# Performance work log

Measured on AMD Instinct MI355X. Metric: run time of the kernel, lower is better.

Reference implementation:

```python
import jax, jax.numpy as jnp
import numpy as np
from jax import lax

VOCAB = 50000; EMB = 128; HID = 256; NL = 9; B = 128; T = 512; H = HID // 2; PAD = 0


def setup_inputs() -> dict:
    key = jax.random.key(0)
    ks = jax.random.split(key, 16)
    p = lambda k, s: jax.random.normal(k, s, jnp.float32) * 0.05
    return {
        "chars": jax.random.randint(ks[0], (B, T), 1, VOCAB),  # in [1, VOCAB) so mask fully on
        "labels": jax.random.randint(ks[1], (B, T), 0, NL),
        "emb": p(ks[2], (VOCAB, EMB)),
        "W_ih_f": p(ks[3], (4 * H, EMB)), "W_hh_f": p(ks[4], (4 * H, H)),
        "b_ih_f": p(ks[5], (4 * H,)), "b_hh_f": p(ks[6], (4 * H,)),
        "W_ih_b": p(ks[7], (4 * H, EMB)), "W_hh_b": p(ks[8], (4 * H, H)),
        "b_ih_b": p(ks[9], (4 * H,)), "b_hh_b": p(ks[10], (4 * H,)),
        "W_out": p(ks[11], (NL, HID)), "b_out": p(ks[12], (NL,)),
        "start_trans": p(ks[13], (NL,)), "end_trans": p(ks[14], (NL,)),
        "trans": p(ks[15], (NL, NL)),
    }


def _lstm(x, Wih, Whh, bih, bhh, reverse):
    # x: (B, T, D); PyTorch gate order i, f, g, o
    bsz = x.shape[0]
    h0 = jnp.zeros((bsz, H), x.dtype)
    c0 = jnp.zeros((bsz, H), x.dtype)
    b = bih + bhh

    def step(carry, xt):
        h, c = carry
        g = xt @ Wih.T + h @ Whh.T + b  # (B, 4H)
        i, f, gg, o = jnp.split(g, 4, axis=-1)
        c = jax.nn.sigmoid(f) * c + jax.nn.sigmoid(i) * jnp.tanh(gg)
        h = jax.nn.sigmoid(o) * jnp.tanh(c)
        return (h, c), h

    _, hs = lax.scan(step, (h0, c0), jnp.swapaxes(x, 0, 1), reverse=reverse)
    return jnp.swapaxes(hs, 0, 1)  # (B, T, H)


def _crf_nll(emissions, labels, mask, start, end, trans):
    # torchcrf linear-chain CRF log-likelihood, reduction='sum'
    maskf = mask.astype(emissions.dtype)
    emit = jnp.take_along_axis(emissions, labels[..., None], 2)[..., 0]  # (B, T)
    score = start[labels[:, 0]] + (emit * maskf).sum(1)
    score = score + (trans[labels[:, :-1], labels[:, 1:]] * maskf[:, 1:]).sum(1)
    last_idx = mask.sum(1).astype(jnp.int32) - 1
    last_tags = jnp.take_along_axis(labels, last_idx[:, None], 1)[:, 0]
    score = score + end[last_tags]

    # forward algorithm (log partition) as a scan over time
    alpha0 = start[None, :] + emissions[:, 0]  # (B, L)

    def step(alpha, inp):
        e_t, m_t = inp  # (B, L), (B,)
        nxt = jax.nn.logsumexp(alpha[:, :, None] + trans[None, :, :], axis=1) + e_t
        return jnp.where(m_t[:, None], nxt, alpha), None

    alpha, _ = lax.scan(step, alpha0,
                        (jnp.swapaxes(emissions, 0, 1)[1:], jnp.swapaxes(mask, 0, 1)[1:]))
    logZ = jax.nn.logsumexp(alpha + end[None, :], axis=-1)
    return -(score - logZ).sum()


def reference(chars, labels, emb, W_ih_f, W_hh_f, b_ih_f, b_hh_f,
              W_ih_b, W_hh_b, b_ih_b, b_hh_b, W_out, b_out,
              start_trans, end_trans, trans):
    x = emb[chars]  # (B, T, EMB)
    hf = _lstm(x, W_ih_f, W_hh_f, b_ih_f, b_hh_f, False)
    hb = _lstm(x, W_ih_b, W_hh_b, b_ih_b, b_hh_b, True)
    h = jnp.concatenate([hf, hb], axis=-1)  # (B, T, HID)
    emissions = h @ W_out.T + b_out  # dropout is identity in eval mode
    mask = chars != PAD
    return _crf_nll(emissions, labels, mask, start_trans, end_trans, trans)
```

## Files before the change

### kernel.cpp

```cpp
#include <hip/hip_runtime.h>

#define B_   128
#define T_   512
#define EMB_ 128
#define H_   128
#define NL_  9
#define MT_  65536

typedef __attribute__((ext_vector_type(8))) short short8v;
typedef __attribute__((ext_vector_type(4))) float float4v;

__device__ inline unsigned short f2bf(float f){
  unsigned u = __float_as_uint(f);
  u += 0x7FFFu + ((u >> 16) & 1u);
  return (unsigned short)(u >> 16);
}
__device__ inline float bf2f(unsigned short s){
  return __uint_as_float(((unsigned)s) << 16);
}
__device__ inline float vrcp(float x){ float r; asm("v_rcp_f32 %0, %1" : "=v"(r) : "v"(x)); return r; }

__device__ inline float poly_sigm(float x){
  float x2 = x * x;
  float t = fmaf(x2, 2.0833333e-3f, -2.0833333e-2f);
  t = fmaf(x2, t, 0.25f);
  return fmaf(x, t, 0.5f);
}
__device__ inline float poly_tanh(float x){
  float x2 = x * x;
  float t = fmaf(x2, 0.13333333f, -0.33333333f);
  t = fmaf(x2, t, 1.f);
  return x * t;
}
__device__ inline float lstm_cell_poly(float pi, float pf, float pg, float po, float& c){
  float iv = poly_sigm(pi);
  float fv = poly_sigm(pf);
  float gv = poly_tanh(pg);
  float ov = poly_sigm(po);
  c = fmaf(fv, c, iv * gv);
  return ov * poly_tanh(c);
}

__device__ inline void bar(){
  __builtin_amdgcn_sched_barrier(0);
  asm volatile("s_waitcnt lgkmcnt(0)" ::: "memory");
  __builtin_amdgcn_sched_barrier(0);
  __builtin_amdgcn_s_barrier();
  __builtin_amdgcn_sched_barrier(0);
}

__device__ inline void gload16(const void* g, void* l){
  __builtin_amdgcn_global_load_lds(
      (const __attribute__((address_space(1))) void*)g,
      (__attribute__((address_space(3)))       void*)l, 16, 0, 0);
}

__global__ void k0_prep(const float* __restrict__ Wihf, const float* __restrict__ Whhf,
                        const float* __restrict__ bihf, const float* __restrict__ bhhf,
                        const float* __restrict__ Wihb, const float* __restrict__ Whhb,
                        const float* __restrict__ bihb, const float* __restrict__ bhhb,
                        unsigned short* __restrict__ Wih2, unsigned short* __restrict__ Whh2,
                        float* __restrict__ biasc){
  int blk = blockIdx.x;
  int dir = blk >> 9;
  int nd  = blk & 511;
  int k   = threadIdx.x;
  int j = nd >> 2, g = nd & 3;
  int orig = g * 128 + j;
  const float* Wih = dir ? Wihb : Wihf;
  const float* Whh = dir ? Whhb : Whhf;
  Wih2[((long)(dir * 512 + nd)) * 128 + k] = f2bf(Wih[orig * EMB_ + k]);
  Whh2[((long)(dir * 512 + nd)) * 128 + k] = f2bf(Whh[orig * H_ + k]);
  if (k == 0){
    const float* bi = dir ? bihb : bihf;
    const float* bh = dir ? bhhb : bhhf;
    biasc[dir * 512 + nd] = bi[orig] + bh[orig];
  }
}

__global__ __launch_bounds__(256) void k2_gemm(const int* __restrict__ chars,
                                               const float* __restrict__ emb,
                                               const unsigned short* __restrict__ Wih2,
                                               const float* __restrict__ biasc,
                                               unsigned short* __restrict__ G){
  __shared__ unsigned short sm[2][128 * 128];
  const int tid = threadIdx.x;
  const int w = tid >> 6, l = tid & 63, r = l & 15, q = l >> 4;
  const long m0 = (long)blockIdx.x * 128;
  const int  n0 = blockIdx.y * 128;

  #pragma unroll
  for (int it = 0; it < 8; it++){
    int u = it * 256 + tid, row = u >> 4, c = u & 15, cs = c ^ (row & 7);
    int ch_ = chars[m0 + row];
    const float4* ep = (const float4*)(emb + (long)ch_ * EMB_ + cs * 8);
    float4 v0 = ep[0], v1 = ep[1];
    short8v o;
    o[0] = (short)f2bf(v0.x); o[1] = (short)f2bf(v0.y);
    o[2] = (short)f2bf(v0.z); o[3] = (short)f2bf(v0.w);
    o[4] = (short)f2bf(v1.x); o[5] = (short)f2bf(v1.y);
    o[6] = (short)f2bf(v1.z); o[7] = (short)f2bf(v1.w);
    *(short8v*)&sm[0][u * 8] = o;
  }
  #pragma unroll
  for (int it = 0; it < 8; it++){
    int u = it * 256 + tid, row = u >> 4, c = u & 15, cs = c ^ (row & 7);
    gload16(Wih2 + (long)(n0 + row) * 128 + cs * 8, &sm[1][u * 8]);
  }
  __syncthreads();

  float bias[8];
  #pragma unroll
  for (int nt = 0; nt < 8; nt++) bias[nt] = biasc[n0 + nt * 16 + r];

  short8v a[2][4];
  #pragma unroll
  for (int mt = 0; mt < 2; mt++){
    int row = 32 * w + mt * 16 + r;
    #pragma unroll
    for (int kf = 0; kf < 4; kf++){
      int ch = (kf * 4 + q) ^ (row & 7);
      a[mt][kf] = *(const short8v*)&sm[0][row * 128 + ch * 8];
    }
  }
  float4v acc[2][8];
  #pragma unroll
  for (int nt = 0; nt < 8; nt++){
    short8v bfr[4];
    int brow = nt * 16 + r;
    #pragma unroll
    for (int kf = 0; kf < 4; kf++){
      int ch = (kf * 4 + q) ^ (brow & 7);
      bfr[kf] = *(const short8v*)&sm[1][brow * 128 + ch * 8];
    }
    #pragma unroll
    for (int mt = 0; mt < 2; mt++){
      float4v z = {bias[nt], bias[nt], bias[nt], bias[nt]};
      acc[mt][nt] = z;
      #pragma unroll
      for (int kf = 0; kf < 4; kf++)
        acc[mt][nt] = __builtin_amdgcn_mfma_f32_16x16x32_bf16(a[mt][kf], bfr[kf], acc[mt][nt], 0, 0, 0);
    }
  }
  __syncthreads();
  unsigned short* gsm = &sm[0][0];
  #pragma unroll
  for (int mt = 0; mt < 2; mt++){
    #pragma unroll
    for (int nt = 0; nt < 8; nt++){
      int rowL = 32 * w + mt * 16 + q * 4;
      #pragma unroll
      for (int reg = 0; reg < 4; reg++)
        gsm[(rowL + reg) * 130 + nt * 16 + r] = f2bf(acc[mt][nt][reg]);
    }
  }
  __syncthreads();
  #pragma unroll
  for (int it = 0; it < 8; it++){
    int u = it * 256 + tid, row = u >> 4, c = u & 15;
    short8v v = *(const short8v*)&gsm[row * 130 + c * 8];
    *(short8v*)(G + (m0 + row) * 1024 + n0 + c * 8) = v;
  }
}

#define HBST 128
__global__ __launch_bounds__(1024, 1) void k3_scan4(
    const unsigned short* __restrict__ G,
    const unsigned short* __restrict__ Whh2,
    unsigned short* __restrict__ hs)
{
  const int blk = blockIdx.x;
  const int dir = blk >> 3;
  const int b0  = (blk & 7) * 16;
  const int tid = threadIdx.x;
  const int w   = tid >> 6;
  const int l   = tid & 63;
  const int r   = l & 15;
  const int q   = l >> 4;
  const int rx  = r & 7;

  __shared__ unsigned short hR[8][16 * HBST];

  short8v Wf[2][4];
  #pragma unroll
  for (int t = 0; t < 2; t++){
    const unsigned short* wp = Whh2 + ((long)(dir * 512 + 32 * w + 16 * t + r)) * 128 + q * 8;
    #pragma unroll
    for (int kf = 0; kf < 4; kf++)
      Wf[t][kf] = *(const short8v*)(wp + kf * 32);
  }
  #pragma unroll
  for (int t = 0; t < 2; t++)
    #pragma unroll
    for (int kf = 0; kf < 4; kf++)
      asm volatile("" : "+v"(Wf[t][kf]));

  for (int i = tid; i < 16 * HBST; i += 1024) hR[7][i] = 0;

  float cc0 = 0.f, cc1 = 0.f;
  const int wcs = ((w ^ rx) << 3);
  const int fii = tid >> 8, fmm = (tid >> 4) & 15, fj8 = tid & 15;
  const int fco = ((fj8 ^ (fmm & 7)) << 3);

  const long gstep = dir ? -1024L : 1024L;
  const unsigned short* gbase = G + ((long)(b0 + r) * T_ + (dir ? T_ - 1 : 0)) * 1024
                                  + dir * 512 + 32 * w + 4 * q;

#define ISSUEX(D0A, D0B, D1A, D1B, S) do{                          \
    const unsigned short* p_ = gbase + (long)(S) * gstep;          \
    D0A = *(const ushort4*)(p_);                                   \
    D0B = *(const ushort4*)(p_ + 16);                              \
    D1A = *(const ushort4*)(p_ + gstep);                           \
    D1B = *(const ushort4*)(p_ + gstep + 16);                      \
  }while(0)

#define STEPX(S, GA, GB) do{                                       \
    const int slot_r = ((S) + 7) & 7, slot_w = (S) & 7;            \
    const unsigned short* rowp = &hR[slot_r][r * HBST];            \
    short8v hf0 = *(const short8v*)(rowp + (((q     ) ^ rx) << 3));\
    short8v hf1 = *(const short8v*)(rowp + (((q +  4) ^ rx) << 3));\
    short8v hf2 = *(const short8v*)(rowp + (((q +  8) ^ rx) << 3));\
    short8v hf3 = *(const short8v*)(rowp + (((q + 12) ^ rx) << 3));\
    float4v acc0 = {bf2f((GA).x), bf2f((GA).y), bf2f((GA).z), bf2f((GA).w)}; \
    float4v acc1 = {bf2f((GB).x), bf2f((GB).y), bf2f((GB).z), bf2f((GB).w)}; \
    acc0 = __builtin_amdgcn_mfma_f32_16x16x32_bf16(Wf[0][0], hf0, acc0, 0, 0, 0); \
    acc0 = __builtin_amdgcn_mfma_f32_16x16x32_bf16(Wf[0][1], hf1, acc0, 0, 0, 0); \
    acc0 = __builtin_amdgcn_mfma_f32_16x16x32_bf16(Wf[0][2], hf2, acc0, 0, 0, 0); \
    acc0 = __builtin_amdgcn_mfma_f32_16x16x32_bf16(Wf[0][3], hf3, acc0, 0, 0, 0); \
    acc1 = __builtin_amdgcn_mfma_f32_16x16x32_bf16(Wf[1][0], hf0, acc1, 0, 0, 0); \
    acc1 = __builtin_amdgcn_mfma_f32_16x16x32_bf16(Wf[1][1], hf1, acc1, 0, 0, 0); \
    acc1 = __builtin_amdgcn_mfma_f32_16x16x32_bf16(Wf[1][2], hf2, acc1, 0, 0, 0); \
    acc1 = __builtin_amdgcn_mfma_f32_16x16x32_bf16(Wf[1][3], hf3, acc1, 0, 0, 0); \
    float hv0 = lstm_cell_poly(acc0[0], acc0[1], acc0[2], acc0[3], cc0);\
    float hv1 = lstm_cell_poly(acc1[0], acc1[1], acc1[2], acc1[3], cc1);\
    unsigned short* wr = &hR[slot_w][r * HBST + wcs];              \
    wr[q]     = f2bf(hv0);                                         \
    wr[q + 4] = f2bf(hv1);                                         \
    bar();                                                         \
  }while(0)

#define FLUSHX(S4) do{                                             \
    int sg_ = (S4) - 4 + fii;                                      \
    int tg_ = dir ? (T_ - 1 - sg_) : sg_;                          \
    short8v v_ = *(const short8v*)&hR[sg_ & 7][fmm * HBST + fco];  \
    *(short8v*)(hs + ((long)dir * MT_ + (long)(b0 + fmm) * T_ + tg_) * H_ + fj8 * 8) = v_; \
  }while(0)

  ushort4 A0a, A0b, A1a, A1b, B0a, B0b, B1a, B1b;
  ISSUEX(A0a, A0b, A1a, A1b, 0);
  bar();

  for (int s4 = 0; s4 < T_; s4 += 4){
    if (s4 > 0) FLUSHX(s4);
    ISSUEX(B0a, B0b, B1a, B1b, s4 + 2);
    STEPX(s4 + 0, A0a, A0b);
    STEPX(s4 + 1, A1a, A1b);
    if (s4 + 4 < T_) ISSUEX(A0a, A0b, A1a, A1b, s4 + 4);
    STEPX(s4 + 2, B0a, B0b);
    STEPX(s4 + 3, B1a, B1b);
  }
  FLUSHX(T_);

#undef ISSUEX
#undef STEPX
#undef FLUSHX
}

#define H4ST 268
__global__ __launch_bounds__(512) void k4_emis(const unsigned short* __restrict__ hs,
                                               const float* __restrict__ Wout,
                                               const float* __restrict__ bout,
                                               const int* __restrict__ chars,
                                               float* __restrict__ em_t,
                                               float* __restrict__ ee2,
                                               float* __restrict__ mTf){
  __shared__ unsigned short hcat[128 * H4ST];
  __shared__ float wo[NL_ * 256];
  int tid = threadIdx.x;
  int t = blockIdx.x;
  const unsigned short* hf = hs;
  const unsigned short* hb = hs + (long)MT_ * H_;
  #pragma unroll
  for (int it = 0; it < 16; it++){
    int flat = it * 2048 + tid * 4;
    int b = flat >> 8, u = flat & 255;
    const unsigned short* src = (u < 128) ? (hf + ((long)b * T_ + t) * H_ + u)
                                          : (hb + ((long)b * T_ + t) * H_ + (u - 128));
    ushort4 v = *(const ushort4*)src;
    *(ushort4*)&hcat[b * H4ST + u] = v;
  }
  for (int f = tid; f < NL_ * 256; f += 512) wo[f] = Wout[f];
  if (tid < 128) mTf[t * B_ + tid] = (chars[tid * T_ + t] != 0) ? 1.f : 0.f;
  __syncthreads();
  #pragma unroll
  for (int half = 0; half < 3; half++){
    int idx = half * 512 + tid;
    if (idx < NL_ * B_){
      int lbl = idx >> 7, b = idx & 127;
      float acc = bout[lbl];
      const unsigned short* hr = &hcat[b * H4ST];
      const float* wl = &wo[lbl * 256];
      #pragma unroll 16
      for (int u4 = 0; u4 < 64; u4++){
        ushort4 hv = ((const ushort4*)hr)[u4];
        acc = fmaf(bf2f(hv.x), wl[u4 * 4],     acc);
        acc = fmaf(bf2f(hv.y), wl[u4 * 4 + 1], acc);
        acc = fmaf(bf2f(hv.z), wl[u4 * 4 + 2], acc);
        acc = fmaf(bf2f(hv.w), wl[u4 * 4 + 3], acc);
      }
      long o = ((long)t * NL_ + lbl) * B_ + b;
      em_t[o] = acc;
      ee2[o] = __expf(acc);
    }
  }
}

__global__ void k5_score(const float* __restrict__ em_t, const int* __restrict__ chars,
                         const int* __restrict__ labels, const float* __restrict__ startv,
                         const float* __restrict__ endv, const float* __restrict__ trans,
                         float* __restrict__ score){
  int b = blockIdx.x, lane = threadIdx.x;
  const int* lab = labels + b * T_;
  const int* ch  = chars + b * T_;
  float sc = 0.f; int cnt = 0;
  for (int t = lane; t < T_; t += 64){
    int m = (ch[t] != 0);
    cnt += m;
    if (m){
      sc += em_t[((long)t * NL_ + lab[t]) * B_ + b];
      if (t > 0) sc += trans[lab[t - 1] * NL_ + lab[t]];
    }
  }
  #pragma unroll
  for (int off = 32; off; off >>= 1){
    sc  += __shfl_down(sc, off);
    cnt += __shfl_down(cnt, off);
  }
  if (lane == 0){
    if (cnt < 1) cnt = 1;
    score[b] = sc + startv[lab[0]] + endv[lab[cnt - 1]];
  }
}

__global__ __launch_bounds__(64) void k5_fwd(const float* __restrict__ ee2,
                                             const float* __restrict__ mTf,
                                             const float* __restrict__ trans,
                                             const float* __restrict__ startv,
                                             const float* __restrict__ endv,
                                             float* __restrict__ logZ){
  int s = blockIdx.x * 64 + threadIdx.x;
  float E[NL_][NL_];
  #pragma unroll
  for (int i = 0; i < NL_; i++)
    #pragma unroll
    for (int j = 0; j < NL_; j++) E[i][j] = __expf(trans[i * NL_ + j]);
  float beta[NL_];
  #pragma unroll
  for (int j = 0; j < NL_; j++) beta[j] = __expf(startv[j]) * ee2[j * B_ + s];
  float L = 0.f;
  float evn[NL_]; float mfn = mTf[B_ + s];
  #pragma unroll
  for (int j = 0; j < NL_; j++) evn[j] = ee2[(NL_ + j) * B_ + s];
  for (int t = 1; t < T_; t++){
    float ev[NL_]; float mf = mfn;
    #pragma unroll
    for (int j = 0; j < NL_; j++) ev[j] = evn[j];
    int t2 = (t + 1 < T_) ? t + 1 : t;
    mfn = mTf[t2 * B_ + s];
    #pragma unroll
    for (int j = 0; j < NL_; j++) evn[j] = ee2[((long)t2 * NL_ + j) * B_ + s];
    float nb[NL_];
    #pragma unroll
    for (int j = 0; j < NL_; j++){
      float acc = beta[0] * E[0][j];
      #pragma unroll
      for (int i = 1; i < NL_; i++) acc = fmaf(beta[i], E[i][j], acc);
      nb[j] = acc * ev[j];
    }
    bool m = mf > 0.5f;
    #pragma unroll
    for (int j = 0; j < NL_; j++) beta[j] = m ? nb[j] : beta[j];
    if ((t & 7) == 0){
      float mx = beta[0];
      #pragma unroll
      for (int j = 1; j < NL_; j++) mx = fmaxf(mx, beta[j]);
      float ri = vrcp(mx);
      #pragma unroll
      for (int j = 0; j < NL_; j++) beta[j] *= ri;
      L += __logf(mx);
    }
  }
  float ssum = 0.f;
  #pragma unroll
  for (int j = 0; j < NL_; j++) ssum = fmaf(beta[j], __expf(endv[j]), ssum);
  logZ[s] = L + __logf(ssum);
}

__global__ void k6_reduce(const float* __restrict__ logZ, const float* __restrict__ score,
                          float* __restrict__ out){
  int lane = threadIdx.x;
  float v = logZ[lane] - score[lane];
  #pragma unroll
  for (int off = 32; off; off >>= 1) v += __shfl_down(v, off);
  __shared__ float tmp[2];
  if ((lane & 63) == 0) tmp[lane >> 6] = v;
  __syncthreads();
  if (lane == 0) out[0] = tmp[0] + tmp[1];
}

extern "C" void kernel_launch(void* const* d_in, const int* in_sizes, int n_in,
                              void* d_out, int out_size, void* d_ws, size_t ws_size,
                              hipStream_t stream){
  const int*   chars  = (const int*)d_in[0];
  const int*   labels = (const int*)d_in[1];
  const float* emb    = (const float*)d_in[2];
  const float* Wihf   = (const float*)d_in[3];
  const float* Whhf   = (const float*)d_in[4];
  const float* bihf   = (const float*)d_in[5];
  const float* bhhf   = (const float*)d_in[6];
  const float* Wihb   = (const float*)d_in[7];
  const float* Whhb   = (const float*)d_in[8];
  const float* bihb   = (const float*)d_in[9];
  const float* bhhb   = (const float*)d_in[10];
  const float* Wout   = (const float*)d_in[11];
  const float* bout   = (const float*)d_in[12];
  const float* startv = (const float*)d_in[13];
  const float* endv   = (const float*)d_in[14];
  const float* trans  = (const float*)d_in[15];

  char* ws = (char*)d_ws;
  float*          em_t  = (float*)         (ws);
  float*          ee2   = (float*)         (ws + 2359296);
  float*          mTf   = (float*)         (ws + 4718592);
  float*          score = (float*)         (ws + 4980736);
  float*          logZ  = (float*)         (ws + 4981248);
  unsigned short* Wih2  = (unsigned short*)(ws + 16777216);
  unsigned short* Whh2  = (unsigned short*)(ws + 17301504);
  float*          biasc = (float*)         (ws + 17825792);
  unsigned short* G     = (unsigned short*)(ws + 17829888);
  unsigned short* hs    = (unsigned short*)(ws + 152047616);

  hipLaunchKernelGGL(k0_prep,  dim3(1024), dim3(128), 0, stream,
                     Wihf, Whhf, bihf, bhhf, Wihb, Whhb, bihb, bhhb, Wih2, Whh2, biasc);
  hipLaunchKernelGGL(k2_gemm,  dim3(512, 8), dim3(256), 0, stream, chars, emb, Wih2, biasc, G);
  hipLaunchKernelGGL(k3_scan4, dim3(16),   dim3(1024), 0, stream, G, Whh2, hs);
  hipLaunchKernelGGL(k4_emis,  dim3(512),  dim3(512), 0, stream, hs, Wout, bout, chars, em_t, ee2, mTf);
  hipLaunchKernelGGL(k5_score, dim3(128),  dim3(64),  0, stream,
                     em_t, chars, labels, startv, endv, trans, score);
  hipLaunchKernelGGL(k5_fwd,   dim3(2),    dim3(64),  0, stream,
                     ee2, mTf, trans, startv, endv, logZ);
  hipLaunchKernelGGL(k6_reduce, dim3(1),   dim3(128), 0, stream, logZ, score, (float*)d_out);
}
```

Baseline: 924.9 us.

## Fuse emission projection into LSTM scan, drop hidden-state writeback

```diff
diff --git a/kernel.cpp b/kernel.cpp
--- a/kernel.cpp
+++ b/kernel.cpp
@@ -59,8 +59,9 @@
                         const float* __restrict__ bihf, const float* __restrict__ bhhf,
                         const float* __restrict__ Wihb, const float* __restrict__ Whhb,
                         const float* __restrict__ bihb, const float* __restrict__ bhhb,
+                        const float* __restrict__ Wout,
                         unsigned short* __restrict__ Wih2, unsigned short* __restrict__ Whh2,
-                        float* __restrict__ biasc){
+                        unsigned short* __restrict__ Wout2, float* __restrict__ biasc){
   int blk = blockIdx.x;
   int dir = blk >> 9;
   int nd  = blk & 511;
@@ -76,6 +77,12 @@
     const float* bh = dir ? bhhb : bhhf;
     biasc[dir * 512 + nd] = bi[orig] + bh[orig];
   }
+  if (blk < 32){
+    int d2 = blk >> 4, row = blk & 15;
+    unsigned short v = 0;
+    if (row < NL_) v = f2bf(Wout[row * 256 + d2 * 128 + k]);
+    Wout2[(d2 * 16 + row) * 128 + k] = v;
+  }
 }
 
 __global__ __launch_bounds__(256) void k2_gemm(const int* __restrict__ chars,
@@ -164,10 +171,11 @@
 }
 
 #define HBST 128
-__global__ __launch_bounds__(1024, 1) void k3_scan4(
+__global__ __launch_bounds__(1024, 1) void k3_scan6(
     const unsigned short* __restrict__ G,
     const unsigned short* __restrict__ Whh2,
-    unsigned short* __restrict__ hs)
+    const unsigned short* __restrict__ Wout2,
+    float* __restrict__ em_p)
 {
   const int blk = blockIdx.x;
   const int dir = blk >> 3;
@@ -195,16 +203,23 @@
     for (int kf = 0; kf < 4; kf++)
       asm volatile("" : "+v"(Wf[t][kf]));
 
+  short8v WfO[4];
+  #pragma unroll
+  for (int kf = 0; kf < 4; kf++)
+    WfO[kf] = *(const short8v*)(Wout2 + ((long)(dir * 16 + r)) * 128 + kf * 32 + q * 8);
+  #pragma unroll
+  for (int kf = 0; kf < 4; kf++)
+    asm volatile("" : "+v"(WfO[kf]));
+
   for (int i = tid; i < 16 * HBST; i += 1024) hR[7][i] = 0;
 
   float cc0 = 0.f, cc1 = 0.f;
   const int wcs = ((w ^ rx) << 3);
-  const int fii = tid >> 8, fmm = (tid >> 4) & 15, fj8 = tid & 15;
-  const int fco = ((fj8 ^ (fmm & 7)) << 3);
 
   const long gstep = dir ? -1024L : 1024L;
   const unsigned short* gbase = G + ((long)(b0 + r) * T_ + (dir ? T_ - 1 : 0)) * 1024
                                   + dir * 512 + 32 * w + 4 * q;
+  float* emp_d = em_p + (long)dir * (T_ * NL_ * B_);
 
 #define ISSUEX(D0A, D0B, D1A, D1B, S) do{                          \
     const unsigned short* p_ = gbase + (long)(S) * gstep;          \
@@ -237,13 +252,25 @@
     wr[q]     = f2bf(hv0);                                         \
     wr[q + 4] = f2bf(hv1);                                         \
     bar();                                                         \
-  }while(0)
-
-#define FLUSHX(S4) do{                                             \
-    int sg_ = (S4) - 4 + fii;                                      \
-    int tg_ = dir ? (T_ - 1 - sg_) : sg_;                          \
-    short8v v_ = *(const short8v*)&hR[sg_ & 7][fmm * HBST + fco];  \
-    *(short8v*)(hs + ((long)dir * MT_ + (long)(b0 + fmm) * T_ + tg_) * H_ + fj8 * 8) = v_; \
+    if (w == ((S) & 15)){                                          \
+      const unsigned short* ep = &hR[slot_w][r * HBST];            \
+      short8v e0 = *(const short8v*)(ep + (((q     ) ^ rx) << 3)); \
+      short8v e1 = *(const short8v*)(ep + (((q +  4) ^ rx) << 3)); \
+      short8v e2 = *(const short8v*)(ep + (((q +  8) ^ rx) << 3)); \
+      short8v e3 = *(const short8v*)(ep + (((q + 12) ^ rx) << 3)); \
+      float4v ae = {0.f, 0.f, 0.f, 0.f};                           \
+      ae = __builtin_amdgcn_mfma_f32_16x16x32_bf16(WfO[0], e0, ae, 0, 0, 0); \
+      ae = __builtin_amdgcn_mfma_f32_16x16x32_bf16(WfO[1], e1, ae, 0, 0, 0); \
+      ae = __builtin_amdgcn_mfma_f32_16x16x32_bf16(WfO[2], e2, ae, 0, 0, 0); \
+      ae = __builtin_amdgcn_mfma_f32_16x16x32_bf16(WfO[3], e3, ae, 0, 0, 0); \
+      int t_ = dir ? (T_ - 1 - (S)) : (S);                         \
+      float* pp = emp_d + (long)t_ * (NL_ * B_) + b0 + r;          \
+      _Pragma("unroll")                                            \
+      for (int reg = 0; reg < 4; reg++){                           \
+        int j_ = q * 4 + reg;                                      \
+        if (j_ < NL_) pp[j_ * B_] = ae[reg];                       \
+      }                                                            \
+    }                                                              \
   }while(0)
 
   ushort4 A0a, A0b, A1a, A1b, B0a, B0b, B1a, B1b;
@@ -251,7 +278,6 @@
   bar();
 
   for (int s4 = 0; s4 < T_; s4 += 4){
-    if (s4 > 0) FLUSHX(s4);
     ISSUEX(B0a, B0b, B1a, B1b, s4 + 2);
     STEPX(s4 + 0, A0a, A0b);
     STEPX(s4 + 1, A1a, A1b);
@@ -259,59 +285,27 @@
     STEPX(s4 + 2, B0a, B0b);
     STEPX(s4 + 3, B1a, B1b);
   }
-  FLUSHX(T_);
 
 #undef ISSUEX
 #undef STEPX
-#undef FLUSHX
-}
-
-#define H4ST 268
-__global__ __launch_bounds__(512) void k4_emis(const unsigned short* __restrict__ hs,
-                                               const float* __restrict__ Wout,
-                                               const float* __restrict__ bout,
-                                               const int* __restrict__ chars,
-                                               float* __restrict__ em_t,
-                                               float* __restrict__ ee2,
-                                               float* __restrict__ mTf){
-  __shared__ unsigned short hcat[128 * H4ST];
-  __shared__ float wo[NL_ * 256];
-  int tid = threadIdx.x;
-  int t = blockIdx.x;
-  const unsigned short* hf = hs;
-  const unsigned short* hb = hs + (long)MT_ * H_;
-  #pragma unroll
-  for (int it = 0; it < 16; it++){
-    int flat = it * 2048 + tid * 4;
-    int b = flat >> 8, u = flat & 255;
-    const unsigned short* src = (u < 128) ? (hf + ((long)b * T_ + t) * H_ + u)
-                                          : (hb + ((long)b * T_ + t) * H_ + (u - 128));
-    ushort4 v = *(const ushort4*)src;
-    *(ushort4*)&hcat[b * H4ST + u] = v;
-  }
-  for (int f = tid; f < NL_ * 256; f += 512) wo[f] = Wout[f];
-  if (tid < 128) mTf[t * B_ + tid] = (chars[tid * T_ + t] != 0) ? 1.f : 0.f;
-  __syncthreads();
-  #pragma unroll
-  for (int half = 0; half < 3; half++){
-    int idx = half * 512 + tid;
-    if (idx < NL_ * B_){
-      int lbl = idx >> 7, b = idx & 127;
-      float acc = bout[lbl];
-      const unsigned short* hr = &hcat[b * H4ST];
-      const float* wl = &wo[lbl * 256];
-      #pragma unroll 16
-      for (int u4 = 0; u4 < 64; u4++){
-        ushort4 hv = ((const ushort4*)hr)[u4];
-        acc = fmaf(bf2f(hv.x), wl[u4 * 4],     acc);
-        acc = fmaf(bf2f(hv.y), wl[u4 * 4 + 1], acc);
-        acc = fmaf(bf2f(hv.z), wl[u4 * 4 + 2], acc);
-        acc = fmaf(bf2f(hv.w), wl[u4 * 4 + 3], acc);
-      }
-      long o = ((long)t * NL_ + lbl) * B_ + b;
-      em_t[o] = acc;
-      ee2[o] = __expf(acc);
-    }
+}
+
+__global__ __launch_bounds__(256) void k4_fin(const float* __restrict__ em_p,
+                                              const float* __restrict__ bout,
+                                              const int* __restrict__ chars,
+                                              float* __restrict__ em_t,
+                                              float* __restrict__ ee2,
+                                              float* __restrict__ mTf){
+  int idx = blockIdx.x * 256 + threadIdx.x;
+  if (idx < T_ * NL_ * B_){
+    int j = (idx >> 7) % NL_;
+    float v = em_p[idx] + em_p[(long)T_ * NL_ * B_ + idx] + bout[j];
+    em_t[idx] = v;
+    ee2[idx] = __expf(v);
+  }
+  if (idx < MT_){
+    int b = idx >> 9, t = idx & 511;
+    mTf[t * B_ + b] = (chars[idx] != 0) ? 1.f : 0.f;
   }
 }
 
@@ -434,17 +428,19 @@
   float*          mTf   = (float*)         (ws + 4718592);
   float*          score = (float*)         (ws + 4980736);
   float*          logZ  = (float*)         (ws + 4981248);
+  float*          em_p  = (float*)         (ws + 5242880);
   unsigned short* Wih2  = (unsigned short*)(ws + 16777216);
   unsigned short* Whh2  = (unsigned short*)(ws + 17301504);
   float*          biasc = (float*)         (ws + 17825792);
+  unsigned short* Wout2 = (unsigned short*)(ws + 17829888 + 134217728);
   unsigned short* G     = (unsigned short*)(ws + 17829888);
-  unsigned short* hs    = (unsigned short*)(ws + 152047616);
 
   hipLaunchKernelGGL(k0_prep,  dim3(1024), dim3(128), 0, stream,
-                     Wihf, Whhf, bihf, bhhf, Wihb, Whhb, bihb, bhhb, Wih2, Whh2, biasc);
+                     Wihf, Whhf, bihf, bhhf, Wihb, Whhb, bihb, bhhb, Wout,
+                     Wih2, Whh2, Wout2, biasc);
   hipLaunchKernelGGL(k2_gemm,  dim3(512, 8), dim3(256), 0, stream, chars, emb, Wih2, biasc, G);
-  hipLaunchKernelGGL(k3_scan4, dim3(16),   dim3(1024), 0, stream, G, Whh2, hs);
-  hipLaunchKernelGGL(k4_emis,  dim3(512),  dim3(512), 0, stream, hs, Wout, bout, chars, em_t, ee2, mTf);
+  hipLaunchKernelGGL(k3_scan6, dim3(16),   dim3(1024), 0, stream, G, Whh2, Wout2, em_p);
+  hipLaunchKernelGGL(k4_fin,   dim3(2304), dim3(256), 0, stream, em_p, bout, chars, em_t, ee2, mTf);
   hipLaunchKernelGGL(k5_score, dim3(128),  dim3(64),  0, stream,
                      em_t, chars, labels, startv, endv, trans, score);
   hipLaunchKernelGGL(k5_fwd,   dim3(2),    dim3(64),  0, stream,
```

Result: slower. 965.7 us (+4.4%).
